# Kernel optimization log

Hardware: AMD Instinct MI355X
Metric: run time of the kernel (lower is better)

The kernel has to match this reference:

```python
import jax, jax.numpy as jnp
import numpy as np

H = 16  # num_heads
EPS = 1e-6

def _sigma(t):
    # ELU(x)+1, the positive feature map used by Infini-attention linear memory
    return jax.nn.elu(t) + 1.0

def setup_inputs() -> dict:
    key = jax.random.key(0)
    ks = jax.random.split(key, 6)
    B, S, D = 1, 2048, 1024
    d = D // H
    std = 1.0 / np.sqrt(D)
    return {
        "x": jax.random.normal(ks[0], (B, S, D), dtype=jnp.float32),
        "M": jnp.zeros((H, d, d), dtype=jnp.float32),
        "z": jnp.zeros((H, d), dtype=jnp.float32),
        "Wq": jax.random.normal(ks[1], (D, D), dtype=jnp.float32) * std,
        "Wk": jax.random.normal(ks[2], (D, D), dtype=jnp.float32) * std,
        "Wv": jax.random.normal(ks[3], (D, D), dtype=jnp.float32) * std,
        "Wo": jax.random.normal(ks[4], (D, D), dtype=jnp.float32) * std,
        "beta": jnp.zeros((H,), dtype=jnp.float32),
    }

def reference(x, M, z, Wq, Wk, Wv, Wo, beta):
    B, S, D = x.shape
    d = D // H
    # projections -> [B, H, S, d]
    def proj(W):
        return (x @ W).reshape(B, S, H, d).transpose(0, 2, 1, 3)
    q, k, v = proj(Wq), proj(Wk), proj(Wv)

    # ---- local causal dot-product attention ----
    scale = 1.0 / jnp.sqrt(jnp.asarray(d, dtype=x.dtype))
    scores = jnp.einsum('bhqd,bhkd->bhqk', q, k) * scale  # [B,H,S,S]
    causal = jnp.tril(jnp.ones((S, S), dtype=bool))
    scores = jnp.where(causal, scores, jnp.asarray(-1e30, dtype=scores.dtype))
    A_dot = jnp.einsum('bhqk,bhkd->bhqd', jax.nn.softmax(scores, axis=-1), v)

    # ---- compressive memory retrieval (linear attention) ----
    sq = _sigma(q)                                       # [B,H,S,d]
    num = jnp.einsum('bhsd,hde->bhse', sq, M)            # [B,H,S,d]
    den = jnp.einsum('bhsd,hd->bhs', sq, z)[..., None]   # [B,H,S,1]
    A_mem = num / (den + EPS)

    # ---- learned gate blend ----
    g = jax.nn.sigmoid(beta).reshape(1, H, 1, 1)
    o = g * A_mem + (1.0 - g) * A_dot                    # [B,H,S,d]
    out = o.transpose(0, 2, 1, 3).reshape(B, S, D) @ Wo  # [B,S,D]

    # ---- memory update (stateful, no_grad in original) ----
    sk = _sigma(k)
    M_new = jax.lax.stop_gradient(M + jnp.einsum('bhsd,bhse->hde', sk, v))
    z_new = jax.lax.stop_gradient(z + sk.sum(axis=(0, 2)))
    return out, M_new, z_new
```

## Files before the change

kernel.cpp:

```cpp
#include <hip/hip_runtime.h>

#define S_LEN 2048
#define D_MODEL 1024
#define NH 16
#define DH 64

typedef __attribute__((ext_vector_type(8))) short bf16x8;
typedef __attribute__((ext_vector_type(4))) float f32x4;

__device__ __forceinline__ f32x4 mfma16(bf16x8 a, bf16x8 b, f32x4 c) {
  return __builtin_amdgcn_mfma_f32_16x16x32_bf16(a, b, c, 0, 0, 0);
}

__device__ __forceinline__ void ldst16(const ushort* g, ushort* l) {
  __builtin_amdgcn_global_load_lds(
      (const __attribute__((address_space(1))) void*)g,
      (__attribute__((address_space(3))) void*)l, 16, 0, 0);
}

__device__ __forceinline__ ushort bf16_rne(float f) {
  unsigned u = __float_as_uint(f);
  unsigned r = (u + 0x7FFFu + ((u >> 16) & 1u)) >> 16;
  return (ushort)r;
}
__device__ __forceinline__ float bf16_to_f(ushort u) {
  return __uint_as_float((unsigned)u << 16);
}

__global__ __launch_bounds__(256) void cast_bf16(
    const float* __restrict__ in, ushort* __restrict__ hi, int n4)
{
  int i = blockIdx.x * 256 + threadIdx.x;
  if (i >= n4) return;
  float4 v = ((const float4*)in)[i];
  ushort4 h;
  h.x = bf16_rne(v.x); h.y = bf16_rne(v.y);
  h.z = bf16_rne(v.z); h.w = bf16_rne(v.w);
  ((ushort4*)hi)[i] = h;
}

__global__ __launch_bounds__(256) void castT(
    const float* __restrict__ W0, const float* __restrict__ W1,
    const float* __restrict__ W2, const float* __restrict__ W3,
    ushort* __restrict__ H0, ushort* __restrict__ H1,
    ushort* __restrict__ H2, ushort* __restrict__ H3)
{
  const int zz = blockIdx.z;
  const float* W = zz == 0 ? W0 : (zz == 1 ? W1 : (zz == 2 ? W2 : W3));
  ushort* H = zz == 0 ? H0 : (zz == 1 ? H1 : (zz == 2 ? H2 : H3));
  __shared__ float ts[32][33];
  const int k0 = blockIdx.x * 32, n0 = blockIdx.y * 32;
  const int r = threadIdx.x >> 3, c4 = (threadIdx.x & 7) * 4;
  float4 v = *(const float4*)&W[(size_t)(k0 + r) * D_MODEL + n0 + c4];
  ts[r][c4 + 0] = v.x; ts[r][c4 + 1] = v.y; ts[r][c4 + 2] = v.z; ts[r][c4 + 3] = v.w;
  __syncthreads();
  ushort4 h;
#pragma unroll
  for (int ii = 0; ii < 4; ii++)
    ((ushort*)&h)[ii] = bf16_rne(ts[c4 + ii][r]);
  *(ushort4*)&H[(size_t)(n0 + r) * D_MODEL + k0 + c4] = h;
}

template<int TM, int TN>
__global__ __launch_bounds__(256, 3) void gemm_h(
    const ushort* __restrict__ Ah,
    const ushort* __restrict__ B0h, const ushort* __restrict__ B1h,
    const ushort* __restrict__ B2h,
    float* __restrict__ C0, int K, int mode,
    ushort* __restrict__ aqb, ushort* __restrict__ akb,
    ushort* __restrict__ akbT, ushort* __restrict__ avbT)
{
  const int t = threadIdx.x;
  const int w = t >> 6, lane = t & 63;
  const int quad = lane >> 4, lr = lane & 15;
  const int bx = blockIdx.x;
  const int bw = (bx * TN) >> 10;
  const int n0 = (bx * TN) & 1023;
  const int m0 = blockIdx.y * TM;
  const ushort* Bh = bw == 0 ? B0h : (bw == 1 ? B1h : B2h);

  __shared__ ushort sAh[TM * 32], sBh[TN * 32];

  constexpr int MF = TM / 32, NF = TN / 32;
  f32x4 acc[MF][NF];
#pragma unroll
  for (int mi = 0; mi < MF; mi++)
#pragma unroll
    for (int ni = 0; ni < NF; ni++)
#pragma unroll
      for (int r = 0; r < 4; r++) acc[mi][ni][r] = 0.f;

  const int mbase = (w & 1) * (TM / 2);
  const int nbase = (w >> 1) * (TN / 2);
  const int rsub = lane >> 2, kcA = (lane & 3) * 8;

  for (int k0 = 0; k0 < K; k0 += 32) {
    __syncthreads();
#pragma unroll
    for (int i = 0; i < TM / 64; i++) {
      int row = i * 64 + w * 16 + rsub;
      ldst16(Ah + (size_t)(m0 + row) * K + k0 + kcA, &sAh[(i * 64 + w * 16) * 32]);
    }
#pragma unroll
    for (int i = 0; i < TN / 64; i++) {
      int row = i * 64 + w * 16 + rsub;
      ldst16(Bh + (size_t)(n0 + row) * K + k0 + kcA, &sBh[(i * 64 + w * 16) * 32]);
    }
    __syncthreads();

    bf16x8 ah[MF], bh[NF];
#pragma unroll
    for (int mi = 0; mi < MF; mi++)
      ah[mi] = *(const bf16x8*)&sAh[(mbase + mi * 16 + lr) * 32 + quad * 8];
#pragma unroll
    for (int ni = 0; ni < NF; ni++)
      bh[ni] = *(const bf16x8*)&sBh[(nbase + ni * 16 + lr) * 32 + quad * 8];
#pragma unroll
    for (int mi = 0; mi < MF; mi++)
#pragma unroll
      for (int ni = 0; ni < NF; ni++)
        acc[mi][ni] = mfma16(ah[mi], bh[ni], acc[mi][ni]);
  }

  if (mode == 0) {
#pragma unroll
    for (int mi = 0; mi < MF; mi++)
#pragma unroll
      for (int ni = 0; ni < NF; ni++)
#pragma unroll
        for (int r = 0; r < 4; r++) {
          int row = m0 + mbase + mi * 16 + quad * 4 + r;
          int col = n0 + nbase + ni * 16 + lr;
          C0[(size_t)row * 1024 + col] = acc[mi][ni][r];
        }
  } else if (bw == 0) {
#pragma unroll
    for (int mi = 0; mi < MF; mi++)
#pragma unroll
      for (int ni = 0; ni < NF; ni++)
#pragma unroll
        for (int r = 0; r < 4; r++) {
          int row = m0 + mbase + mi * 16 + quad * 4 + r;
          int col = n0 + nbase + ni * 16 + lr;
          aqb[(size_t)row * 1024 + col] = bf16_rne(acc[mi][ni][r] * 0.125f);
        }
  } else if (bw == 1) {
#pragma unroll
    for (int mi = 0; mi < MF; mi++)
#pragma unroll
      for (int ni = 0; ni < NF; ni++) {
        int row0 = m0 + mbase + mi * 16 + quad * 4;
        int col = n0 + nbase + ni * 16 + lr;
        ushort4 pk;
#pragma unroll
        for (int r = 0; r < 4; r++) {
          ushort b = bf16_rne(acc[mi][ni][r]);
          ((ushort*)&pk)[r] = b;
          akb[(size_t)(row0 + r) * 1024 + col] = b;
        }
        *(ushort4*)&akbT[(size_t)col * 2048 + row0] = pk;
      }
  } else {
#pragma unroll
    for (int mi = 0; mi < MF; mi++)
#pragma unroll
      for (int ni = 0; ni < NF; ni++) {
        int row0 = m0 + mbase + mi * 16 + quad * 4;
        int col = n0 + nbase + ni * 16 + lr;
        ushort4 pk;
#pragma unroll
        for (int r = 0; r < 4; r++)
          ((ushort*)&pk)[r] = bf16_rne(acc[mi][ni][r]);
        *(ushort4*)&avbT[(size_t)col * 2048 + row0] = pk;
      }
  }
}

__global__ __launch_bounds__(256, 3) void attn_fused(
    const ushort* __restrict__ qb, const ushort* __restrict__ kb,
    const ushort* __restrict__ vbT, const ushort* __restrict__ kbT,
    const float* __restrict__ Mmem, const float* __restrict__ zmem,
    const float* __restrict__ beta,
    ushort* __restrict__ oh,
    float* __restrict__ Mout, float* __restrict__ zout)
{
  const int t = threadIdx.x;
  const int w = t >> 6, lane = t & 63;
  const int quad = lane >> 4, lr = lane & 15;

  __shared__ __align__(16) ushort sBuf[24576];
  __shared__ float drow[64];
  __shared__ float sL[64];

  if (blockIdx.x < 16) {
    const int h = blockIdx.x;
    float* red = (float*)sBuf;
    f32x4 acc[4][4];
#pragma unroll
    for (int mt = 0; mt < 4; mt++)
#pragma unroll
      for (int nt = 0; nt < 4; nt++)
#pragma unroll
        for (int r = 0; r < 4; r++) acc[mt][nt][r] = 0.f;
    float accZ[4] = {0.f, 0.f, 0.f, 0.f};

#pragma unroll 2
    for (int step = 0; step < 16; step++) {
      int k0 = w * 512 + step * 32;
      bf16x8 ah[4], al[4];
#pragma unroll
      for (int mt = 0; mt < 4; mt++) {
        bf16x8 raw = *(const bf16x8*)&kbT[(size_t)(h * 64 + mt * 16 + lr) * 2048 + k0 + quad * 8];
        bf16x8 hh, ll;
#pragma unroll
        for (int j = 0; j < 8; j++) {
          float f = bf16_to_f((ushort)raw[j]);
          float s = f > 0.f ? f + 1.f : __expf(f);
          accZ[mt] += s;
          ushort hb = bf16_rne(s);
          hh[j] = (short)hb;
          ll[j] = (short)bf16_rne(s - bf16_to_f(hb));
        }
        ah[mt] = hh; al[mt] = ll;
      }
      bf16x8 bv[4];
#pragma unroll
      for (int nt = 0; nt < 4; nt++)
        bv[nt] = *(const bf16x8*)&vbT[(size_t)(h * 64 + nt * 16 + lr) * 2048 + k0 + quad * 8];
#pragma unroll
      for (int mt = 0; mt < 4; mt++)
#pragma unroll
        for (int nt = 0; nt < 4; nt++) {
          acc[mt][nt] = mfma16(ah[mt], bv[nt], acc[mt][nt]);
          acc[mt][nt] = mfma16(al[mt], bv[nt], acc[mt][nt]);
        }
    }
#pragma unroll
    for (int mt = 0; mt < 4; mt++) {
      accZ[mt] += __shfl_xor(accZ[mt], 16);
      accZ[mt] += __shfl_xor(accZ[mt], 32);
    }
    if (w < 2) {
#pragma unroll
      for (int mt = 0; mt < 4; mt++)
#pragma unroll
        for (int nt = 0; nt < 4; nt++)
#pragma unroll
          for (int r = 0; r < 4; r++)
            red[w * 4096 + (mt * 16 + quad * 4 + r) * 64 + nt * 16 + lr] = acc[mt][nt][r];
    }
    __syncthreads();
    if (w >= 2) {
#pragma unroll
      for (int mt = 0; mt < 4; mt++)
#pragma unroll
        for (int nt = 0; nt < 4; nt++)
#pragma unroll
          for (int r = 0; r < 4; r++)
            red[(w - 2) * 4096 + (mt * 16 + quad * 4 + r) * 64 + nt * 16 + lr] += acc[mt][nt][r];
    }
    __syncthreads();
    for (int i = t; i < 4096; i += 256)
      Mout[(size_t)h * 4096 + i] = Mmem[(size_t)h * 4096 + i] + red[i] + red[4096 + i];
    __syncthreads();
    if (quad == 0) {
#pragma unroll
      for (int mt = 0; mt < 4; mt++)
        red[w * 64 + mt * 16 + lr] = accZ[mt];
    }
    __syncthreads();
    if (t < 64)
      zout[h * 64 + t] = zmem[h * 64 + t] + red[t] + red[64 + t] + red[128 + t] + red[192 + t];
    return;
  }

  const int a  = blockIdx.x - 16;
  const int h  = a >> 5;
  const int p  = (a >> 1) & 15;
  const int qt = (a & 1) ? p : 31 - p;
  const int s0 = qt * 64;
  const int ntiles = (qt + 2) >> 1;

  const int SPQ = 0, SK = 8192, SVT = 16384;

#pragma unroll
  for (int i = 0; i < 2; i++) {
    int li = w * 2 + i;
    int row = li * 8 + (lane >> 3);
    int cg = ((lane & 7) - row) & 7;
    ldst16(qb + (size_t)(s0 + row) * 1024 + h * 64 + cg * 8, &sBuf[SPQ + li * 512]);
  }
  __syncthreads();
  const int arow = w * 16 + lr;
  const bf16x8 aq0 = *(const bf16x8*)&sBuf[SPQ + arow * 64 + ((quad + arow) & 7) * 8];
  const bf16x8 aq1 = *(const bf16x8*)&sBuf[SPQ + arow * 64 + ((4 + quad + arow) & 7) * 8];

  f32x4 oaccT[4];
#pragma unroll
  for (int ni = 0; ni < 4; ni++)
#pragma unroll
    for (int r = 0; r < 4; r++) oaccT[ni][r] = 0.f;
  f32x4 lacc;
#pragma unroll
  for (int r = 0; r < 4; r++) lacc[r] = 0.f;
  bf16x8 aone;
#pragma unroll
  for (int j = 0; j < 8; j++) aone[j] = (short)0x3F80;

  for (int jt = 0; jt < ntiles; jt++) {
    const int j0 = jt * 128;
    __syncthreads();
#pragma unroll
    for (int i = 0; i < 4; i++) {
      int li = w * 4 + i;
      int rowK = li * 8 + (lane >> 3);
      int cgK = ((lane & 7) - rowK) & 7;
      ldst16(kb + (size_t)(j0 + rowK) * 1024 + h * 64 + cgK * 8,
             &sBuf[SK + li * 512]);
      int rowV = li * 4 + (lane >> 4);
      int cgV = ((lane & 15) - rowV) & 15;
      ldst16(vbT + (size_t)(h * 64 + rowV) * 2048 + j0 + cgV * 8,
             &sBuf[SVT + li * 512]);
    }
    __syncthreads();

    f32x4 sc[8];
#pragma unroll
    for (int nj = 0; nj < 8; nj++) {
      int brow = nj * 16 + lr;
      bf16x8 b0 = *(const bf16x8*)&sBuf[SK + brow * 64 + ((quad + brow) & 7) * 8];
      bf16x8 b1 = *(const bf16x8*)&sBuf[SK + brow * 64 + ((4 + quad + brow) & 7) * 8];
      f32x4 z4; z4[0] = z4[1] = z4[2] = z4[3] = 0.f;
      z4 = mfma16(b0, aq0, z4);
      sc[nj] = mfma16(b1, aq1, z4);
    }
    if (jt == ntiles - 1) {
#pragma unroll
      for (int nj = 0; nj < 8; nj++)
#pragma unroll
        for (int r = 0; r < 4; r++)
          if (j0 + nj * 16 + quad * 4 + r > s0 + arow) sc[nj][r] = -1e30f;
    }

#pragma unroll
    for (int nj = 0; nj < 8; nj++) {
      ushort4 pk;
#pragma unroll
      for (int r = 0; r < 4; r++) {
        float e = exp2f(fmaf(sc[nj][r], 1.4426950408889634f, -23.083120654223414f));
        ((ushort*)&pk)[r] = bf16_rne(e);
      }
      int col = nj * 16 + quad * 4;
      *(ushort4*)&sBuf[SPQ + arow * 128 + ((col + arow * 8) & 127)] = pk;
    }

#pragma unroll
    for (int kf = 0; kf < 4; kf++) {
      bf16x8 bp = *(const bf16x8*)&sBuf[SPQ + arow * 128 + ((kf * 32 + quad * 8 + arow * 8) & 127)];
#pragma unroll
      for (int ni = 0; ni < 4; ni++) {
        int vrow = ni * 16 + lr;
        bf16x8 av = *(const bf16x8*)&sBuf[SVT + vrow * 128 + ((kf * 32 + quad * 8 + vrow * 8) & 127)];
        oaccT[ni] = mfma16(av, bp, oaccT[ni]);
      }
      lacc = mfma16(aone, bp, lacc);
    }
  }
  __syncthreads();

  float* sF  = (float*)sBuf;
  float* sO  = sF;
  float* ssq = sF + 4352;
  if (quad == 0) sL[arow] = lacc[0];
#pragma unroll
  for (int ni = 0; ni < 4; ni++) {
    float4 o4 = make_float4(oaccT[ni][0], oaccT[ni][1], oaccT[ni][2], oaccT[ni][3]);
    *(float4*)&sO[arow * 68 + ni * 16 + quad * 4] = o4;
  }

#pragma unroll
  for (int i = 0; i < 4; i++) {
    int idx4 = t + i * 256;
    int r = idx4 >> 4, c4 = (idx4 & 15) * 4;
    ushort4 u4 = *(const ushort4*)&qb[(size_t)(s0 + r) * 1024 + h * 64 + c4];
#pragma unroll
    for (int j = 0; j < 4; j++) {
      float qv = bf16_to_f(((const ushort*)&u4)[j]) * 8.0f;
      ssq[(c4 + j) * 68 + r] = qv > 0.f ? qv + 1.f : __expf(qv);
    }
  }
  __syncthreads();

  {
    int rr2 = t >> 2, part = t & 3;
    float ds = 0.f;
#pragma unroll
    for (int jj = 0; jj < 16; jj++) {
      int c = part + jj * 4;
      ds = fmaf(ssq[c * 68 + rr2], zmem[h * 64 + c], ds);
    }
    ds += __shfl_xor(ds, 1);
    ds += __shfl_xor(ds, 2);
    if (part == 0) drow[rr2] = ds + 1e-6f;
  }
  __syncthreads();

  const int tx = t & 15, ty = t >> 4;
  float nacc[4][4] = {};
#pragma unroll 8
  for (int dd = 0; dd < 64; dd++) {
    float4 av = *(const float4*)&ssq[dd * 68 + ty * 4];
    float4 bv = *(const float4*)&Mmem[(size_t)h * 4096 + dd * 64 + tx * 4];
    float aa[4] = {av.x, av.y, av.z, av.w};
    float bb[4] = {bv.x, bv.y, bv.z, bv.w};
#pragma unroll
    for (int i = 0; i < 4; i++)
#pragma unroll
      for (int j = 0; j < 4; j++)
        nacc[i][j] = fmaf(aa[i], bb[j], nacc[i][j]);
  }
  float g = 1.f / (1.f + __expf(-beta[h]));
#pragma unroll
  for (int i = 0; i < 4; i++) {
    int r = ty * 4 + i;
    float invd = g / drow[r];
    float invl = (1.f - g) / sL[r];
    float4 od = *(const float4*)&sO[r * 68 + tx * 4];
    float b0 = nacc[i][0] * invd + od.x * invl;
    float b1 = nacc[i][1] * invd + od.y * invl;
    float b2 = nacc[i][2] * invd + od.z * invl;
    float b3 = nacc[i][3] * invd + od.w * invl;
    ushort4 hh;
    hh.x = bf16_rne(b0); hh.y = bf16_rne(b1);
    hh.z = bf16_rne(b2); hh.w = bf16_rne(b3);
    *(ushort4*)&oh[(size_t)(s0 + r) * 1024 + h * 64 + tx * 4] = hh;
  }
}

extern "C" void kernel_launch(void* const* d_in, const int* in_sizes, int n_in,
                              void* d_out, int out_size, void* d_ws, size_t ws_size,
                              hipStream_t stream) {
  const float* x    = (const float*)d_in[0];
  const float* M    = (const float*)d_in[1];
  const float* z    = (const float*)d_in[2];
  const float* Wq   = (const float*)d_in[3];
  const float* Wk   = (const float*)d_in[4];
  const float* Wv   = (const float*)d_in[5];
  const float* Wo   = (const float*)d_in[6];
  const float* beta = (const float*)d_in[7];

  float* out  = (float*)d_out;
  float* Mout = out + (size_t)S_LEN * D_MODEL;
  float* zout = Mout + NH*DH*DH;

  const size_t NE = (size_t)S_LEN * D_MODEL;
  const size_t WE = (size_t)D_MODEL * D_MODEL;
  ushort* xh  = (ushort*)d_ws;
  ushort* wqh = xh + NE;
  ushort* wkh = wqh + WE;
  ushort* wvh = wkh + WE;
  ushort* woh = wvh + WE;
  ushort* qb  = woh + WE;
  ushort* kb  = qb + NE;
  ushort* kbT = kb + NE;
  ushort* vbT = kbT + NE;
  ushort* ohb = vbT + NE;

  cast_bf16<<<dim3(NE/4/256), 256, 0, stream>>>(x, xh, (int)(NE/4));
  castT<<<dim3(32, 32, 4), 256, 0, stream>>>(Wq, Wk, Wv, Wo,
      wqh, wkh, wvh, woh);

  gemm_h<128, 128><<<dim3(24, 16), 256, 0, stream>>>(xh,
      wqh, wkh, wvh,
      (float*)nullptr, D_MODEL, 1, qb, kb, kbT, vbT);

  attn_fused<<<dim3(528), 256, 0, stream>>>(qb, kb, vbT, kbT,
      M, z, beta, ohb, Mout, zout);

  gemm_h<64, 128><<<dim3(8, 32), 256, 0, stream>>>(ohb,
      woh, woh, woh,
      out, D_MODEL, 0, nullptr, nullptr, nullptr, nullptr);
}
```

Measured before the change: 182.3 us.

## Merge cast kernels into one launch and double GEMM K-step to 64

Combines the x-to-bf16 cast and the weight transpose-cast into a single prep kernel, removing one kernel launch. The GEMM now stages 64-wide K slices in LDS instead of 32, so each tile does half as many barrier pairs and two MFMA sub-steps per load. The price is doubled LDS per block, which may limit occupancy against the launch_bounds(256,3) target, and LDS row strides of 64 elements that may cause more bank conflicts.

```diff
diff --git a/kernel.cpp b/kernel.cpp
--- a/kernel.cpp
+++ b/kernel.cpp
@@ -27,29 +27,29 @@
   return __uint_as_float((unsigned)u << 16);
 }
 
-__global__ __launch_bounds__(256) void cast_bf16(
-    const float* __restrict__ in, ushort* __restrict__ hi, int n4)
-{
-  int i = blockIdx.x * 256 + threadIdx.x;
-  if (i >= n4) return;
-  float4 v = ((const float4*)in)[i];
-  ushort4 h;
-  h.x = bf16_rne(v.x); h.y = bf16_rne(v.y);
-  h.z = bf16_rne(v.z); h.w = bf16_rne(v.w);
-  ((ushort4*)hi)[i] = h;
-}
-
-__global__ __launch_bounds__(256) void castT(
+__global__ __launch_bounds__(256) void prep(
+    const float* __restrict__ x, ushort* __restrict__ xh,
     const float* __restrict__ W0, const float* __restrict__ W1,
     const float* __restrict__ W2, const float* __restrict__ W3,
     ushort* __restrict__ H0, ushort* __restrict__ H1,
     ushort* __restrict__ H2, ushort* __restrict__ H3)
 {
-  const int zz = blockIdx.z;
+  int b = blockIdx.x;
+  if (b < 2048) {
+    int i = b * 256 + threadIdx.x;
+    float4 v = ((const float4*)x)[i];
+    ushort4 h;
+    h.x = bf16_rne(v.x); h.y = bf16_rne(v.y);
+    h.z = bf16_rne(v.z); h.w = bf16_rne(v.w);
+    ((ushort4*)xh)[i] = h;
+    return;
+  }
+  b -= 2048;
+  const int zz = b >> 10;
   const float* W = zz == 0 ? W0 : (zz == 1 ? W1 : (zz == 2 ? W2 : W3));
   ushort* H = zz == 0 ? H0 : (zz == 1 ? H1 : (zz == 2 ? H2 : H3));
   __shared__ float ts[32][33];
-  const int k0 = blockIdx.x * 32, n0 = blockIdx.y * 32;
+  const int k0 = (b & 31) * 32, n0 = ((b >> 5) & 31) * 32;
   const int r = threadIdx.x >> 3, c4 = (threadIdx.x & 7) * 4;
   float4 v = *(const float4*)&W[(size_t)(k0 + r) * D_MODEL + n0 + c4];
   ts[r][c4 + 0] = v.x; ts[r][c4 + 1] = v.y; ts[r][c4 + 2] = v.z; ts[r][c4 + 3] = v.w;
@@ -79,7 +79,7 @@
   const int m0 = blockIdx.y * TM;
   const ushort* Bh = bw == 0 ? B0h : (bw == 1 ? B1h : B2h);
 
-  __shared__ ushort sAh[TM * 32], sBh[TN * 32];
+  __shared__ ushort sAh[TM * 64], sBh[TN * 64];
 
   constexpr int MF = TM / 32, NF = TN / 32;
   f32x4 acc[MF][NF];
@@ -92,34 +92,37 @@
 
   const int mbase = (w & 1) * (TM / 2);
   const int nbase = (w >> 1) * (TN / 2);
-  const int rsub = lane >> 2, kcA = (lane & 3) * 8;
-
-  for (int k0 = 0; k0 < K; k0 += 32) {
-    __syncthreads();
-#pragma unroll
-    for (int i = 0; i < TM / 64; i++) {
-      int row = i * 64 + w * 16 + rsub;
-      ldst16(Ah + (size_t)(m0 + row) * K + k0 + kcA, &sAh[(i * 64 + w * 16) * 32]);
-    }
-#pragma unroll
-    for (int i = 0; i < TN / 64; i++) {
-      int row = i * 64 + w * 16 + rsub;
-      ldst16(Bh + (size_t)(n0 + row) * K + k0 + kcA, &sBh[(i * 64 + w * 16) * 32]);
-    }
-    __syncthreads();
-
-    bf16x8 ah[MF], bh[NF];
-#pragma unroll
-    for (int mi = 0; mi < MF; mi++)
-      ah[mi] = *(const bf16x8*)&sAh[(mbase + mi * 16 + lr) * 32 + quad * 8];
-#pragma unroll
-    for (int ni = 0; ni < NF; ni++)
-      bh[ni] = *(const bf16x8*)&sBh[(nbase + ni * 16 + lr) * 32 + quad * 8];
-#pragma unroll
-    for (int mi = 0; mi < MF; mi++)
+  const int r8 = lane >> 3, kc = (lane & 7) * 8;
+
+  for (int k0 = 0; k0 < K; k0 += 64) {
+    __syncthreads();
+#pragma unroll
+    for (int i = 0; i < TM / 32; i++) {
+      int row0 = (w * (TM / 32) + i) * 8;
+      ldst16(Ah + (size_t)(m0 + row0 + r8) * K + k0 + kc, &sAh[row0 * 64]);
+    }
+#pragma unroll
+    for (int i = 0; i < TN / 32; i++) {
+      int row0 = (w * (TN / 32) + i) * 8;
+      ldst16(Bh + (size_t)(n0 + row0 + r8) * K + k0 + kc, &sBh[row0 * 64]);
+    }
+    __syncthreads();
+
+#pragma unroll
+    for (int kk = 0; kk < 2; kk++) {
+      bf16x8 ah[MF], bh[NF];
+#pragma unroll
+      for (int mi = 0; mi < MF; mi++)
+        ah[mi] = *(const bf16x8*)&sAh[(mbase + mi * 16 + lr) * 64 + kk * 32 + quad * 8];
 #pragma unroll
       for (int ni = 0; ni < NF; ni++)
-        acc[mi][ni] = mfma16(ah[mi], bh[ni], acc[mi][ni]);
+        bh[ni] = *(const bf16x8*)&sBh[(nbase + ni * 16 + lr) * 64 + kk * 32 + quad * 8];
+#pragma unroll
+      for (int mi = 0; mi < MF; mi++)
+#pragma unroll
+        for (int ni = 0; ni < NF; ni++)
+          acc[mi][ni] = mfma16(ah[mi], bh[ni], acc[mi][ni]);
+    }
   }
 
   if (mode == 0) {
@@ -466,8 +469,7 @@
   ushort* vbT = kbT + NE;
   ushort* ohb = vbT + NE;
 
-  cast_bf16<<<dim3(NE/4/256), 256, 0, stream>>>(x, xh, (int)(NE/4));
-  castT<<<dim3(32, 32, 4), 256, 0, stream>>>(Wq, Wk, Wv, Wo,
+  prep<<<dim3(2048 + 4096), 256, 0, stream>>>(x, xh, Wq, Wk, Wv, Wo,
       wqh, wkh, wvh, woh);
 
   gemm_h<128, 128><<<dim3(24, 16), 256, 0, stream>>>(xh,
```

Measured after the change: 183.1 us. Within noise of the previous version (+0.5%).
